# Kernel tuning notes

Hardware: AMD Instinct MI355X
Metric: run time of the kernel (lower is better)

Reference implementation:

```python
import jax, jax.numpy as jnp
import numpy as np

KERNEL_MUL = 2.0
KERNEL_NUM = 5


def setup_inputs() -> dict:
    key = jax.random.key(0)
    k1, k2 = jax.random.split(key)
    source = jax.random.normal(k1, (4096, 256), dtype=jnp.float32)
    target = jax.random.normal(k2, (4096, 256), dtype=jnp.float32)
    return {"source": source, "target": target}


def _mmd(source, target):
    b = source.shape[0]
    total = jnp.concatenate([source, target], axis=0)  # [N, D], N = 2b
    n = total.shape[0]
    sq = jnp.sum(total * total, axis=-1)               # [N]
    gram = total @ total.T                             # [N, N]
    L2 = sq[:, None] + sq[None, :] - 2.0 * gram        # [N, N]
    # Data-dependent bandwidth (original uses .data -> no grad through it)
    bandwidth = jax.lax.stop_gradient(jnp.sum(L2) / (n * n - n))
    # Multi-bandwidth RBF kernel, averaged over KERNEL_NUM geometric sigmas.
    kernels = jnp.zeros_like(L2)
    for i in range(KERNEL_NUM):
        sigma = bandwidth * (KERNEL_MUL ** i)
        kernels = kernels + jnp.exp(-L2 / sigma)
    kernels = kernels / KERNEL_NUM
    XX = kernels[:b, :b]
    YY = kernels[b:, b:]
    XY = kernels[:b, b:]
    YX = kernels[b:, :b]
    return jnp.mean(XX + YY - XY - YX)


def reference(source, target):
    return _mmd(source, target)
```

## Files before the change

### kernel.cpp

```cpp
#include <hip/hip_runtime.h>
#include <hip/hip_bf16.h>

#define N_TOTAL 8192
#define B_HALF  4096
#define D       256
#define BM      128
#define BK      64
#define NTILES  (N_TOTAL / BM)
#define NBLK    (NTILES * (NTILES + 1) / 2)
#define NPAIR   (NBLK / 2)
#define PREP_BLOCKS (N_TOTAL / 32)

typedef __bf16 bf16x8v __attribute__((ext_vector_type(8)));
typedef float  f32x4v  __attribute__((ext_vector_type(4)));

__device__ __forceinline__ unsigned short f2bf(float x) {
    unsigned int u = __float_as_uint(x);
    return (unsigned short)((u + 0x7FFFu + ((u >> 16) & 1u)) >> 16);
}
__device__ __forceinline__ float bf2f(unsigned short b) {
    return __uint_as_float(((unsigned int)b) << 16);
}

__device__ __forceinline__ void gload_lds16(const void* g, void* l) {
    __builtin_amdgcn_global_load_lds(
        (const __attribute__((address_space(1))) unsigned int*)g,
        (__attribute__((address_space(3))) unsigned int*)l,
        16, 0, 0);
}

__global__ void prep_kernel(const float* __restrict__ src,
                            const float* __restrict__ tgt,
                            unsigned short* __restrict__ tb,
                            float* __restrict__ sq,
                            float* __restrict__ colsum_part,
                            double* __restrict__ sumsq_part)
{
    __shared__ float colpart[4][256];
    __shared__ double wsum[4];
    int tid = threadIdx.x;
    int wv = tid >> 6, ln = tid & 63;
    int row0 = blockIdx.x * 32 + wv * 8;

    float cp0 = 0.f, cp1 = 0.f, cp2 = 0.f, cp3 = 0.f;
    double dsum = 0.0;

    for (int t = 0; t < 8; ++t) {
        int row = row0 + t;
        const float* p = (row < B_HALF) ? (src + (size_t)row * D)
                                        : (tgt + (size_t)(row - B_HALF) * D);
        float4 v = *(const float4*)(p + ln * 4);
        unsigned short b0 = f2bf(v.x), b1 = f2bf(v.y), b2 = f2bf(v.z), b3 = f2bf(v.w);
        float x0 = bf2f(b0), x1 = bf2f(b1), x2 = bf2f(b2), x3 = bf2f(b3);
        ushort4 u; u.x = b0; u.y = b1; u.z = b2; u.w = b3;
        *(ushort4*)(tb + (size_t)row * D + ln * 4) = u;

        cp0 += x0; cp1 += x1; cp2 += x2; cp3 += x3;

        float sqp = x0 * x0 + x1 * x1 + x2 * x2 + x3 * x3;
        #pragma unroll
        for (int off = 32; off; off >>= 1) sqp += __shfl_down(sqp, off, 64);
        if (ln == 0) { sq[row] = sqp; dsum += (double)sqp; }
    }
    colpart[wv][ln * 4 + 0] = cp0;
    colpart[wv][ln * 4 + 1] = cp1;
    colpart[wv][ln * 4 + 2] = cp2;
    colpart[wv][ln * 4 + 3] = cp3;
    if (ln == 0) wsum[wv] = dsum;
    __syncthreads();
    colsum_part[blockIdx.x * 256 + tid] =
        colpart[0][tid] + colpart[1][tid] + colpart[2][tid] + colpart[3][tid];
    if (tid == 0)
        sumsq_part[blockIdx.x] = wsum[0] + wsum[1] + wsum[2] + wsum[3];
}

__global__ void bw_kernel(const float* __restrict__ colsum_part,
                          const double* __restrict__ sumsq_part,
                          float* __restrict__ cexp) {
    __shared__ double red1[256], red2[256];
    int tid = threadIdx.x;
    float cs = 0.f;
    for (int b = 0; b < PREP_BLOCKS; ++b)
        cs += colsum_part[b * 256 + tid];
    red1[tid] = sumsq_part[tid];
    red2[tid] = (double)cs * (double)cs;
    __syncthreads();
    for (int off = 128; off; off >>= 1) {
        if (tid < off) { red1[tid] += red1[tid + off]; red2[tid] += red2[tid + off]; }
        __syncthreads();
    }
    if (tid == 0) {
        double sl2 = 2.0 * (double)N_TOTAL * red1[0] - 2.0 * red2[0];
        double bw = sl2 / ((double)N_TOTAL * N_TOTAL - (double)N_TOTAL);
        cexp[0] = (float)(1.4426950408889634 / (16.0 * bw));
    }
}

__device__ __forceinline__ void stage_tiles(const unsigned short* __restrict__ tb,
                                            int rowBase, int colBase, int kb0,
                                            int wv, int ln,
                                            unsigned short* ldsA,
                                            unsigned short* ldsB) {
    #pragma unroll
    for (int i = 0; i < 4; ++i) {
        int o = i * 4096 + wv * 1024 + ln * 16;
        int rowl = o >> 7;
        int colb = (o & 127) ^ ((rowl & 7) << 4);
        gload_lds16(tb + (size_t)(rowBase + rowl) * D + kb0 + (colb >> 1),
                    (char*)ldsA + i * 4096 + wv * 1024);
        gload_lds16(tb + (size_t)(colBase + rowl) * D + kb0 + (colb >> 1),
                    (char*)ldsB + i * 4096 + wv * 1024);
    }
}

__global__ __launch_bounds__(256, 2)
void mmd_kernel(const unsigned short* __restrict__ tb,
                const float* __restrict__ sq,
                const float* __restrict__ cexp_p,
                double* __restrict__ partials) {
    __shared__ __align__(16) unsigned short lds[2][2][BM * BK];
    __shared__ float sqi[2][BM], sqj[2][BM];
    __shared__ float redbuf[4];

    int t0 = blockIdx.x * 2;
    int r0 = (int)((sqrtf(8.0f * (float)t0 + 1.0f) - 1.0f) * 0.5f);
    while ((r0 + 1) * (r0 + 2) / 2 <= t0) ++r0;
    while (r0 * (r0 + 1) / 2 > t0) --r0;
    int c0 = t0 - r0 * (r0 + 1) / 2;
    int r1 = r0, c1 = c0 + 1;
    if (c1 > r0) { r1 = r0 + 1; c1 = 0; }

    const int rowB[2] = {r0 * BM, r1 * BM};
    const int colB[2] = {c0 * BM, c1 * BM};
    float wt[2];
    wt[0] = (((r0 < NTILES / 2) == (c0 < NTILES / 2)) ? 1.f : -1.f) * (r0 != c0 ? 2.f : 1.f);
    wt[1] = (((r1 < NTILES / 2) == (c1 < NTILES / 2)) ? 1.f : -1.f) * (r1 != c1 ? 2.f : 1.f);

    int tid = threadIdx.x;
    int wv = tid >> 6, ln = tid & 63;
    int wr = wv >> 1, wc = wv & 1;
    int lo = ln & 15, hi = ln >> 4;

    stage_tiles(tb, rowB[0], colB[0], 0, wv, ln, lds[0][0], lds[0][1]);

    if (tid < BM) { sqi[0][tid] = sq[rowB[0] + tid]; sqi[1][tid] = sq[rowB[1] + tid]; }
    else { int u = tid - BM; sqj[0][u] = sq[colB[0] + u]; sqj[1][u] = sq[colB[1] + u]; }
    float cexp = cexp_p[0];

    __syncthreads();

    f32x4v acc[4][4] = {};
    float tacc = 0.f;

    #pragma unroll
    for (int s = 0; s < 8; ++s) {
        const int cur = s & 1;
        const int tile = s >> 2;

        if (s < 7) {
            const int tn = (s + 1) >> 2, kn = (s + 1) & 3;
            stage_tiles(tb, rowB[tn], colB[tn], kn * BK, wv, ln,
                        lds[cur ^ 1][0], lds[cur ^ 1][1]);
            __builtin_amdgcn_sched_barrier(0);
        }

        bf16x8v a[2][4], b[2][4];
        #pragma unroll
        for (int kk = 0; kk < 2; ++kk) {
            #pragma unroll
            for (int mi = 0; mi < 4; ++mi) {
                int rowl = wr * 64 + mi * 16 + lo;
                int colb = (kk * 64 + hi * 16) ^ ((rowl & 7) << 4);
                a[kk][mi] = *(const bf16x8v*)((const char*)lds[cur][0] + rowl * 128 + colb);
            }
            #pragma unroll
            for (int ni = 0; ni < 4; ++ni) {
                int rowl = wc * 64 + ni * 16 + lo;
                int colb = (kk * 64 + hi * 16) ^ ((rowl & 7) << 4);
                b[kk][ni] = *(const bf16x8v*)((const char*)lds[cur][1] + rowl * 128 + colb);
            }
        }

        __builtin_amdgcn_s_setprio(1);
        #pragma unroll
        for (int kk = 0; kk < 2; ++kk)
            #pragma unroll
            for (int mi = 0; mi < 4; ++mi)
                #pragma unroll
                for (int ni = 0; ni < 4; ++ni)
                    acc[mi][ni] = __builtin_amdgcn_mfma_f32_16x16x32_bf16(
                        a[kk][mi], b[kk][ni], acc[mi][ni], 0, 0, 0);
        __builtin_amdgcn_s_setprio(0);

        if ((s & 3) == 3) {
            float ep = 0.f;
            #pragma unroll
            for (int mi = 0; mi < 4; ++mi) {
                float si4[4];
                #pragma unroll
                for (int rg = 0; rg < 4; ++rg)
                    si4[rg] = sqi[tile][wr * 64 + mi * 16 + hi * 4 + rg];
                #pragma unroll
                for (int ni = 0; ni < 4; ++ni) {
                    float sj = sqj[tile][wc * 64 + ni * 16 + lo];
                    #pragma unroll
                    for (int rg = 0; rg < 4; ++rg) {
                        float arg = (2.0f * acc[mi][ni][rg] - (si4[rg] + sj)) * cexp;
                        float e0 = __builtin_amdgcn_exp2f(arg);
                        float e2 = e0 * e0, e4 = e2 * e2, e8 = e4 * e4, e16 = e8 * e8;
                        ep += (e0 + e2) + ((e4 + e8) + e16);
                    }
                }
            }
            tacc += wt[tile] * ep;
            #pragma unroll
            for (int mi = 0; mi < 4; ++mi)
                #pragma unroll
                for (int ni = 0; ni < 4; ++ni)
                    acc[mi][ni] = f32x4v{0.f, 0.f, 0.f, 0.f};
        }

        if (s < 7) {
            asm volatile("s_waitcnt vmcnt(0)" ::: "memory");
            __builtin_amdgcn_s_barrier();
        }
    }

    #pragma unroll
    for (int off = 32; off; off >>= 1) tacc += __shfl_down(tacc, off, 64);
    if (ln == 0) redbuf[wv] = tacc;
    __syncthreads();
    if (tid == 0)
        partials[blockIdx.x] =
            (double)(redbuf[0] + redbuf[1] + redbuf[2] + redbuf[3]);
}

__global__ void final_kernel(const double* __restrict__ partials,
                             float* __restrict__ out) {
    __shared__ double dred[256];
    int tid = threadIdx.x;
    double d = 0.0;
    for (int i = tid; i < NPAIR; i += 256) d += partials[i];
    dred[tid] = d;
    __syncthreads();
    for (int off = 128; off; off >>= 1) {
        if (tid < off) dred[tid] += dred[tid + off];
        __syncthreads();
    }
    if (tid == 0)
        out[0] = (float)(dred[0] / (5.0 * (double)B_HALF * (double)B_HALF));
}

extern "C" void kernel_launch(void* const* d_in, const int* in_sizes, int n_in,
                              void* d_out, int out_size, void* d_ws, size_t ws_size,
                              hipStream_t stream) {
    const float* src = (const float*)d_in[0];
    const float* tgt = (const float*)d_in[1];
    float* out = (float*)d_out;
    char* ws = (char*)d_ws;

    float*  cexp     = (float*)(ws + 16);
    double* ssqpart  = (double*)(ws + 2048);
    float*  sq       = (float*)(ws + 4096);
    double* partials = (double*)(ws + 36864);
    float*  cspart   = (float*)(ws + 131072);
    unsigned short* tb = (unsigned short*)(ws + 1048576);

    prep_kernel<<<PREP_BLOCKS, 256, 0, stream>>>(src, tgt, tb, sq, cspart,
                                                 ssqpart);
    bw_kernel<<<1, 256, 0, stream>>>(cspart, ssqpart, cexp);
    mmd_kernel<<<NPAIR, 256, 0, stream>>>(tb, sq, cexp, partials);
    final_kernel<<<1, 256, 0, stream>>>(partials, out);
}
```

Baseline: 59.39 us.

## Split each 128x128 tile across eight waves instead of four

New measurement: 67.48 us. +13.6%, slower.

```diff
diff --git a/kernel.cpp b/kernel.cpp
--- a/kernel.cpp
+++ b/kernel.cpp
@@ -80,6 +80,7 @@
     __shared__ double red1[256], red2[256];
     int tid = threadIdx.x;
     float cs = 0.f;
+    #pragma unroll 4
     for (int b = 0; b < PREP_BLOCKS; ++b)
         cs += colsum_part[b * 256 + tid];
     red1[tid] = sumsq_part[tid];
@@ -98,29 +99,29 @@
 
 __device__ __forceinline__ void stage_tiles(const unsigned short* __restrict__ tb,
                                             int rowBase, int colBase, int kb0,
-                                            int wv, int ln,
+                                            int wid, int ln,
                                             unsigned short* ldsA,
                                             unsigned short* ldsB) {
     #pragma unroll
-    for (int i = 0; i < 4; ++i) {
-        int o = i * 4096 + wv * 1024 + ln * 16;
+    for (int i = 0; i < 2; ++i) {
+        int o = i * 8192 + wid * 1024 + ln * 16;
         int rowl = o >> 7;
         int colb = (o & 127) ^ ((rowl & 7) << 4);
         gload_lds16(tb + (size_t)(rowBase + rowl) * D + kb0 + (colb >> 1),
-                    (char*)ldsA + i * 4096 + wv * 1024);
+                    (char*)ldsA + i * 8192 + wid * 1024);
         gload_lds16(tb + (size_t)(colBase + rowl) * D + kb0 + (colb >> 1),
-                    (char*)ldsB + i * 4096 + wv * 1024);
-    }
-}
-
-__global__ __launch_bounds__(256, 2)
+                    (char*)ldsB + i * 8192 + wid * 1024);
+    }
+}
+
+__global__ __launch_bounds__(512, 4)
 void mmd_kernel(const unsigned short* __restrict__ tb,
                 const float* __restrict__ sq,
                 const float* __restrict__ cexp_p,
                 double* __restrict__ partials) {
     __shared__ __align__(16) unsigned short lds[2][2][BM * BK];
     __shared__ float sqi[2][BM], sqj[2][BM];
-    __shared__ float redbuf[4];
+    __shared__ float redbuf[8];
 
     int t0 = blockIdx.x * 2;
     int r0 = (int)((sqrtf(8.0f * (float)t0 + 1.0f) - 1.0f) * 0.5f);
@@ -137,19 +138,21 @@
     wt[1] = (((r1 < NTILES / 2) == (c1 < NTILES / 2)) ? 1.f : -1.f) * (r1 != c1 ? 2.f : 1.f);
 
     int tid = threadIdx.x;
-    int wv = tid >> 6, ln = tid & 63;
-    int wr = wv >> 1, wc = wv & 1;
+    int wid = tid >> 6, ln = tid & 63;
+    int wr = wid >> 1, wc = wid & 1;
     int lo = ln & 15, hi = ln >> 4;
 
-    stage_tiles(tb, rowB[0], colB[0], 0, wv, ln, lds[0][0], lds[0][1]);
-
-    if (tid < BM) { sqi[0][tid] = sq[rowB[0] + tid]; sqi[1][tid] = sq[rowB[1] + tid]; }
-    else { int u = tid - BM; sqj[0][u] = sq[colB[0] + u]; sqj[1][u] = sq[colB[1] + u]; }
+    stage_tiles(tb, rowB[0], colB[0], 0, wid, ln, lds[0][0], lds[0][1]);
+
+    if (tid < BM)            sqi[0][tid]       = sq[rowB[0] + tid];
+    else if (tid < 2 * BM)   sqj[0][tid - BM]  = sq[colB[0] + (tid - BM)];
+    else if (tid < 3 * BM)   sqi[1][tid - 256] = sq[rowB[1] + (tid - 256)];
+    else                     sqj[1][tid - 384] = sq[colB[1] + (tid - 384)];
     float cexp = cexp_p[0];
 
     __syncthreads();
 
-    f32x4v acc[4][4] = {};
+    f32x4v acc[2][4] = {};
     float tacc = 0.f;
 
     #pragma unroll
@@ -159,17 +162,17 @@
 
         if (s < 7) {
             const int tn = (s + 1) >> 2, kn = (s + 1) & 3;
-            stage_tiles(tb, rowB[tn], colB[tn], kn * BK, wv, ln,
+            stage_tiles(tb, rowB[tn], colB[tn], kn * BK, wid, ln,
                         lds[cur ^ 1][0], lds[cur ^ 1][1]);
             __builtin_amdgcn_sched_barrier(0);
         }
 
-        bf16x8v a[2][4], b[2][4];
+        bf16x8v a[2][2], b[2][4];
         #pragma unroll
         for (int kk = 0; kk < 2; ++kk) {
             #pragma unroll
-            for (int mi = 0; mi < 4; ++mi) {
-                int rowl = wr * 64 + mi * 16 + lo;
+            for (int mi = 0; mi < 2; ++mi) {
+                int rowl = wr * 32 + mi * 16 + lo;
                 int colb = (kk * 64 + hi * 16) ^ ((rowl & 7) << 4);
                 a[kk][mi] = *(const bf16x8v*)((const char*)lds[cur][0] + rowl * 128 + colb);
             }
@@ -185,7 +188,7 @@
         #pragma unroll
         for (int kk = 0; kk < 2; ++kk)
             #pragma unroll
-            for (int mi = 0; mi < 4; ++mi)
+            for (int mi = 0; mi < 2; ++mi)
                 #pragma unroll
                 for (int ni = 0; ni < 4; ++ni)
                     acc[mi][ni] = __builtin_amdgcn_mfma_f32_16x16x32_bf16(
@@ -195,11 +198,11 @@
         if ((s & 3) == 3) {
             float ep = 0.f;
             #pragma unroll
-            for (int mi = 0; mi < 4; ++mi) {
+            for (int mi = 0; mi < 2; ++mi) {
                 float si4[4];
                 #pragma unroll
                 for (int rg = 0; rg < 4; ++rg)
-                    si4[rg] = sqi[tile][wr * 64 + mi * 16 + hi * 4 + rg];
+                    si4[rg] = sqi[tile][wr * 32 + mi * 16 + hi * 4 + rg];
                 #pragma unroll
                 for (int ni = 0; ni < 4; ++ni) {
                     float sj = sqj[tile][wc * 64 + ni * 16 + lo];
@@ -214,7 +217,7 @@
             }
             tacc += wt[tile] * ep;
             #pragma unroll
-            for (int mi = 0; mi < 4; ++mi)
+            for (int mi = 0; mi < 2; ++mi)
                 #pragma unroll
                 for (int ni = 0; ni < 4; ++ni)
                     acc[mi][ni] = f32x4v{0.f, 0.f, 0.f, 0.f};
@@ -228,11 +231,14 @@
 
     #pragma unroll
     for (int off = 32; off; off >>= 1) tacc += __shfl_down(tacc, off, 64);
-    if (ln == 0) redbuf[wv] = tacc;
-    __syncthreads();
-    if (tid == 0)
-        partials[blockIdx.x] =
-            (double)(redbuf[0] + redbuf[1] + redbuf[2] + redbuf[3]);
+    if (ln == 0) redbuf[wid] = tacc;
+    __syncthreads();
+    if (tid == 0) {
+        float bsum = 0.f;
+        #pragma unroll
+        for (int w = 0; w < 8; ++w) bsum += redbuf[w];
+        partials[blockIdx.x] = (double)bsum;
+    }
 }
 
 __global__ void final_kernel(const double* __restrict__ partials,
@@ -269,6 +275,6 @@
     prep_kernel<<<PREP_BLOCKS, 256, 0, stream>>>(src, tgt, tb, sq, cspart,
                                                  ssqpart);
     bw_kernel<<<1, 256, 0, stream>>>(cspart, ssqpart, cexp);
-    mmd_kernel<<<NPAIR, 256, 0, stream>>>(tb, sq, cexp, partials);
+    mmd_kernel<<<NPAIR, 512, 0, stream>>>(tb, sq, cexp, partials);
     final_kernel<<<1, 256, 0, stream>>>(partials, out);
 }
```
